# Kernel tuning notes

Measured on AMD Instinct MI355X. Metric: run time of the kernel, lower is better.

Reference implementation:

```python
import jax, jax.numpy as jnp
import numpy as np

B, N, T, H = 64, 15, 256, 128
TEMP = 1.0


def setup_inputs() -> dict:
    key = jax.random.key(0)
    ks = jax.random.split(key, 5)
    node_output = jax.random.normal(ks[0], (B, T, H), jnp.float32)
    neigh_output = jax.random.normal(ks[1], (B, N, T, H), jnp.float32)
    # causal-style mask: True = masked (t' > t); guarantees no fully-masked row
    attn_mask = jnp.broadcast_to(jnp.triu(jnp.ones((T, T), bool), k=1), (B, T, T))
    xav = (2.0 / (H + H)) ** 0.5  # xavier_normal std for square HxH
    Wq = jax.random.normal(ks[2], (H, H), jnp.float32) * xav
    Wk = jax.random.normal(ks[3], (H, H), jnp.float32) * xav
    Wv = jax.random.normal(ks[4], (H, H), jnp.float32) * xav
    z = jnp.zeros((H,), jnp.float32)  # biases init to 0 in init_params
    return dict(node_output=node_output, neigh_output=neigh_output,
                neighbors_number=N, attn_mask=attn_mask,
                Wq=Wq, bq=z, Wk=Wk, bk=z, Wv=Wv, bv=z)


def reference(node_output, neigh_output, neighbors_number, attn_mask,
              Wq, bq, Wk, bk, Wv, bv):
    b, t, h = node_output.shape
    n = neigh_output.shape[1]
    # key/value sequence: self node followed by its n neighbors -> [B, N+1, T, H]
    kv = jnp.concatenate([node_output[:, None], neigh_output], axis=1)
    # Linear (torch convention y = x W^T + b); query repeat collapses to single proj
    q = node_output @ Wq.T + bq                      # [B, T, H]
    k = kv @ Wk.T + bk                               # [B, N+1, T, H]
    v = kv.reshape(b, (n + 1) * t, h) @ Wv.T + bv    # [B, (N+1)*T, H]
    # scores: each query attends separately to every (source, timestep) key
    S = jnp.einsum('bth,bnsh->bnts', q, k)           # [B, N+1, T, T]
    # S_norm computed on the PRE-mask scores (original norms S.data before fill)
    S_norm = jnp.linalg.norm(S.reshape(b, -1), axis=-1)  # [B]
    S = jnp.where(attn_mask[:, None, :, :], -jnp.inf, S)
    S = jnp.transpose(S, (0, 2, 1, 3)) / TEMP        # [B, T, N+1, T]
    # joint softmax over all (N+1)*T keys at once
    A = jax.nn.softmax(S.reshape(b, t, (n + 1) * t), axis=-1)
    out = jnp.einsum('btk,bkh->bth', A, v)           # [B, T, H]
    return out, A.reshape(b, t, n + 1, t), S_norm
```

## Files before the change

### kernel.cpp

```cpp
#include <hip/hip_runtime.h>
#include <math.h>


constexpr int BB   = 64;
constexpr int TT   = 256;
constexpr int HH   = 128;
constexpr int KEYS = 4096;
constexpr int LDK  = 136;
constexpr int LDV  = 72;

typedef __attribute__((ext_vector_type(8)))  __bf16 bf16x8;
typedef __attribute__((ext_vector_type(16))) float  f32x16;
typedef unsigned short ushort_t;

__device__ __forceinline__ float4 ld4(const float* p) {
  return *reinterpret_cast<const float4*>(p);
}
__device__ __forceinline__ ushort_t f2bf(float x) {
  union { __bf16 b; ushort_t u; } c; c.b = (__bf16)x; return c.u;
}
__device__ __forceinline__ float bf2f(ushort_t h) {
  return __uint_as_float(((unsigned)h) << 16);
}
__device__ __forceinline__ void splitf(float x, ushort_t& h, ushort_t& l) {
  h = f2bf(x);
  l = f2bf(x - bf2f(h));
}
__device__ __forceinline__ f32x16 zero16() {
  f32x16 z;
  #pragma unroll
  for (int i = 0; i < 16; ++i) z[i] = 0.f;
  return z;
}
__device__ __forceinline__ f32x16 mfma3(bf16x8 ahi, bf16x8 alo,
                                        bf16x8 bhi, bf16x8 blo, f32x16 c) {
  c = __builtin_amdgcn_mfma_f32_32x32x16_bf16(ahi, bhi, c, 0, 0, 0);
  c = __builtin_amdgcn_mfma_f32_32x32x16_bf16(ahi, blo, c, 0, 0, 0);
  c = __builtin_amdgcn_mfma_f32_32x32x16_bf16(alo, bhi, c, 0, 0, 0);
  return c;
}

__global__ __launch_bounds__(256) void prep_w_kernel(
    const float* __restrict__ Wq, const float* __restrict__ Wk,
    const float* __restrict__ Wv,
    ushort_t* __restrict__ wqh, ushort_t* __restrict__ wql,
    ushort_t* __restrict__ wkh, ushort_t* __restrict__ wkl,
    ushort_t* __restrict__ wvh, ushort_t* __restrict__ wvl)
{
  int i = blockIdx.x * 256 + threadIdx.x;
  if (i >= HH * HH) return;
  ushort_t h, l;
  splitf(Wq[i], h, l); wqh[i] = h; wql[i] = l;
  splitf(Wk[i], h, l); wkh[i] = h; wkl[i] = l;
  splitf(Wv[i], h, l); wvh[i] = h; wvl[i] = l;
}

template<bool DOV>
__global__ __launch_bounds__(256, 2) void proj_kernel(
    const float* __restrict__ node, const float* __restrict__ neigh,
    const ushort_t* __restrict__ W1h, const ushort_t* __restrict__ W1l,
    const float* __restrict__ b1,
    const ushort_t* __restrict__ WVh, const ushort_t* __restrict__ WVl,
    const float* __restrict__ bV,
    ushort_t* __restrict__ yh, ushort_t* __restrict__ yl,
    ushort_t* __restrict__ v_t, int mode)
{
  __shared__ ushort_t xh[128 * LDK];
  __shared__ ushort_t xl[128 * LDK];
  const int tid = threadIdx.x;
  const long r0 = (long)blockIdx.x * 128;

  #pragma unroll
  for (int i = 0; i < 16; ++i) {
    int slot = tid + 256 * i;
    int row = slot >> 5, h0 = (slot & 31) << 2;
    long r = r0 + row;
    const float* src;
    if (mode == 0) {
      src = node + r * HH;
    } else {
      long bb = r >> 12;
      int  n  = (int)((r >> 8) & 15);
      int  t  = (int)(r & 255);
      src = (n == 0) ? (node + (bb * TT + t) * HH)
                     : (neigh + ((bb * 15 + (n - 1)) * (long)TT + t) * HH);
    }
    float4 xv = ld4(src + h0);
    ushort_t h0h, h0l, h1h, h1l, h2h, h2l, h3h, h3l;
    splitf(xv.x, h0h, h0l); splitf(xv.y, h1h, h1l);
    splitf(xv.z, h2h, h2l); splitf(xv.w, h3h, h3l);
    *reinterpret_cast<uint2*>(&xh[row * LDK + h0]) =
        make_uint2((unsigned)h0h | ((unsigned)h1h << 16),
                   (unsigned)h2h | ((unsigned)h3h << 16));
    *reinterpret_cast<uint2*>(&xl[row * LDK + h0]) =
        make_uint2((unsigned)h0l | ((unsigned)h1l << 16),
                   (unsigned)h2l | ((unsigned)h3l << 16));
  }
  __syncthreads();

  const int l = tid & 63, w = tid >> 6, g = l >> 5, lane31 = l & 31;
  const int j = 32 * w + lane31;

  f32x16 accK[4];
  #pragma unroll
  for (int kt = 0; kt < 4; ++kt) accK[kt] = zero16();
  f32x16 accV[4];
  if constexpr (DOV) {
    #pragma unroll
    for (int kt = 0; kt < 4; ++kt) accV[kt] = zero16();
  }

  #pragma unroll
  for (int hs = 0; hs < 8; ++hs) {
    const int ho = 16 * hs + 8 * g;
    bf16x8 wh = *reinterpret_cast<const bf16x8*>(W1h + j * HH + ho);
    bf16x8 wl = *reinterpret_cast<const bf16x8*>(W1l + j * HH + ho);
    bf16x8 xhf[4], xlf[4];
    #pragma unroll
    for (int rt = 0; rt < 4; ++rt) {
      xhf[rt] = *reinterpret_cast<const bf16x8*>(&xh[(32 * rt + lane31) * LDK + ho]);
      xlf[rt] = *reinterpret_cast<const bf16x8*>(&xl[(32 * rt + lane31) * LDK + ho]);
    }
    #pragma unroll
    for (int rt = 0; rt < 4; ++rt)
      accK[rt] = mfma3(xhf[rt], xlf[rt], wh, wl, accK[rt]);
    if constexpr (DOV) {
      bf16x8 vh = *reinterpret_cast<const bf16x8*>(WVh + j * HH + ho);
      bf16x8 vl = *reinterpret_cast<const bf16x8*>(WVl + j * HH + ho);
      #pragma unroll
      for (int rt = 0; rt < 4; ++rt)
        accV[rt] = mfma3(vh, vl, xhf[rt], xlf[rt], accV[rt]);
    }
  }

  const float bK = b1[j];
  #pragma unroll
  for (int kt = 0; kt < 4; ++kt) {
    #pragma unroll
    for (int reg = 0; reg < 16; ++reg) {
      int rm = (reg & 3) + 8 * (reg >> 2) + 4 * g;
      long r = r0 + 32 * kt + rm;
      ushort_t h, lo_;
      splitf(accK[kt][reg] + bK, h, lo_);
      yh[r * HH + j] = h;
      yl[r * HH + j] = lo_;
    }
  }
  if constexpr (DOV) {
    const int bidx = (int)(r0 >> 12);
    const int key0 = (int)(r0 & (KEYS - 1));
    float bvr[16];
    #pragma unroll
    for (int reg = 0; reg < 16; ++reg)
      bvr[reg] = bV[32 * w + (reg & 3) + 8 * (reg >> 2) + 4 * g];
    #pragma unroll
    for (int kt = 0; kt < 4; ++kt) {
      #pragma unroll
      for (int reg = 0; reg < 16; ++reg) {
        int rm = (reg & 3) + 8 * (reg >> 2) + 4 * g;
        int jrow = 32 * w + rm;
        v_t[((long)(bidx * HH + jrow)) * KEYS + key0 + 32 * kt + lane31] =
            f2bf(accV[kt][reg] + bvr[reg]);
      }
    }
  }
}

__global__ __launch_bounds__(128, 2) void passA_kernel(
    const ushort_t* __restrict__ q_hi, const ushort_t* __restrict__ q_lo,
    const ushort_t* __restrict__ k_hi, const ushort_t* __restrict__ k_lo,
    float* __restrict__ m_part, float* __restrict__ l_part,
    float* __restrict__ ssq_part)
{
  __shared__ ushort_t Khi[64 * LDK];
  __shared__ ushort_t Klo[64 * LDK];
  const int tid = threadIdx.x, l = tid & 63, w = tid >> 6;
  const int g = (l >> 5) & 1, lane31 = l & 31;
  const int p = blockIdx.x;
  const int xcd = p & 7, slot = p >> 3;
  const int pair = xcd * 32 + (slot >> 2);
  const int tq = slot & 3;
  const int b = pair >> 2, ks = pair & 3;
  const int t0 = tq * 64;

  bf16x8 qhi[8], qlo[8];
  {
    const long qb = ((long)(b * TT + t0 + 32 * w + lane31)) * HH;
    #pragma unroll
    for (int hs = 0; hs < 8; ++hs) {
      qhi[hs] = *reinterpret_cast<const bf16x8*>(q_hi + qb + 16 * hs + 8 * g);
      qlo[hs] = *reinterpret_cast<const bf16x8*>(q_lo + qb + 16 * hs + 8 * g);
    }
  }

  float mreg[16], lreg[16], ssq = 0.f;
  #pragma unroll
  for (int r = 0; r < 16; ++r) { mreg[r] = -1e30f; lreg[r] = 0.f; }

  for (int kt = 0; kt < 16; ++kt) {
    const int kb = ks * 1024 + kt * 64;
    __syncthreads();
    #pragma unroll
    for (int i = 0; i < 8; ++i) {
      int slot2 = i * 128 + tid;
      int row = slot2 >> 4, c0 = (slot2 & 15) << 3;
      const long gsrc = ((long)(b * KEYS + kb + row)) * HH + c0;
      *reinterpret_cast<uint4*>(&Khi[row * LDK + c0]) =
          *reinterpret_cast<const uint4*>(k_hi + gsrc);
      *reinterpret_cast<uint4*>(&Klo[row * LDK + c0]) =
          *reinterpret_cast<const uint4*>(k_lo + gsrc);
    }
    __syncthreads();

    f32x16 acc0 = zero16(), acc1 = zero16();
    #pragma unroll
    for (int hs = 0; hs < 8; ++hs) {
      const int ho = 16 * hs + 8 * g;
      bf16x8 kh0 = *reinterpret_cast<const bf16x8*>(&Khi[lane31 * LDK + ho]);
      bf16x8 kl0 = *reinterpret_cast<const bf16x8*>(&Klo[lane31 * LDK + ho]);
      bf16x8 kh1 = *reinterpret_cast<const bf16x8*>(&Khi[(32 + lane31) * LDK + ho]);
      bf16x8 kl1 = *reinterpret_cast<const bf16x8*>(&Klo[(32 + lane31) * LDK + ho]);
      acc0 = mfma3(qhi[hs], qlo[hs], kh0, kl0, acc0);
      acc1 = mfma3(qhi[hs], qlo[hs], kh1, kl1, acc1);
    }

    const int st0 = (kb + lane31) & 255;
    const int st1 = (kb + 32 + lane31) & 255;
    #pragma unroll
    for (int reg = 0; reg < 16; ++reg) {
      const int tr = t0 + 32 * w + (reg & 3) + 8 * (reg >> 2) + 4 * g;
      float s0 = acc0[reg], s1 = acc1[reg];
      ssq = fmaf(s0, s0, fmaf(s1, s1, ssq));
      bool msk0 = st0 > tr, msk1 = st1 > tr;
      float v0 = msk0 ? -1e30f : s0;
      float v1 = msk1 ? -1e30f : s1;
      float mn = fmaxf(mreg[reg], fmaxf(v0, v1));
      float sc = __expf(mreg[reg] - mn);
      float p0 = msk0 ? 0.f : __expf(s0 - mn);
      float p1 = msk1 ? 0.f : __expf(s1 - mn);
      lreg[reg] = fmaf(lreg[reg], sc, p0 + p1);
      mreg[reg] = mn;
    }
  }

  #pragma unroll
  for (int reg = 0; reg < 16; ++reg) {
    #pragma unroll
    for (int off = 1; off < 32; off <<= 1) {
      float mo = __shfl_xor(mreg[reg], off);
      float lo = __shfl_xor(lreg[reg], off);
      float mn = fmaxf(mreg[reg], mo);
      lreg[reg] = lreg[reg] * __expf(mreg[reg] - mn) + lo * __expf(mo - mn);
      mreg[reg] = mn;
    }
  }
  if (lane31 == 0) {
    #pragma unroll
    for (int reg = 0; reg < 16; ++reg) {
      const int tr = t0 + 32 * w + (reg & 3) + 8 * (reg >> 2) + 4 * g;
      m_part[ks * (BB * TT) + b * TT + tr] = mreg[reg];
      l_part[ks * (BB * TT) + b * TT + tr] = lreg[reg];
    }
  }
  #pragma unroll
  for (int off = 1; off < 64; off <<= 1) ssq += __shfl_xor(ssq, off);
  __syncthreads();
  float* red = reinterpret_cast<float*>(Khi);
  if (l == 0) red[w] = ssq;
  __syncthreads();
  if (tid == 0) ssq_part[b * 16 + tq * 4 + ks] = red[0] + red[1];
}

__global__ void merge_ml_kernel(const float* __restrict__ m_part,
                                const float* __restrict__ l_part,
                                float* __restrict__ m_ws,
                                float* __restrict__ l_ws)
{
  int idx = blockIdx.x * 256 + threadIdx.x;
  if (idx >= BB * TT) return;
  float m = -1e30f;
  #pragma unroll
  for (int k = 0; k < 4; ++k) m = fmaxf(m, m_part[k * (BB * TT) + idx]);
  float lsum = 0.f;
  #pragma unroll
  for (int k = 0; k < 4; ++k)
    lsum += l_part[k * (BB * TT) + idx] * __expf(m_part[k * (BB * TT) + idx] - m);
  m_ws[idx] = m;
  l_ws[idx] = lsum;
}

__global__ __launch_bounds__(256, 2) void passB_kernel(
    const ushort_t* __restrict__ q_hi, const ushort_t* __restrict__ q_lo,
    const ushort_t* __restrict__ k_hi, const ushort_t* __restrict__ k_lo,
    const ushort_t* __restrict__ v_t,
    const float* __restrict__ m_ws, const float* __restrict__ l_ws,
    float* __restrict__ A_out, float* __restrict__ opart)
{
  __shared__ ushort_t Khi[64 * LDK];
  __shared__ ushort_t Klo[64 * LDK];
  __shared__ ushort_t Vt[128 * LDV];
  __shared__ ushort_t As[64 * LDV];
  const int tid = threadIdx.x, l = tid & 63, w = tid >> 6;
  const int g = (l >> 5) & 1, lane31 = l & 31;
  const int wt = w & 1, wk = w >> 1;
  const int p = blockIdx.x;
  const int xcd = p & 7, slot = p >> 3;
  const int pair = xcd * 16 + (slot >> 2);
  const int tq = slot & 3;
  const int b = pair >> 1, ksb = pair & 1;
  const int t0 = tq * 64;

  bf16x8 qhi[8], qlo[8];
  {
    const long qb = ((long)(b * TT + t0 + 32 * wt + lane31)) * HH;
    #pragma unroll
    for (int hs = 0; hs < 8; ++hs) {
      qhi[hs] = *reinterpret_cast<const bf16x8*>(q_hi + qb + 16 * hs + 8 * g);
      qlo[hs] = *reinterpret_cast<const bf16x8*>(q_lo + qb + 16 * hs + 8 * g);
    }
  }
  float mreg[16], rinv[16];
  #pragma unroll
  for (int reg = 0; reg < 16; ++reg) {
    const int tr = t0 + 32 * wt + (reg & 3) + 8 * (reg >> 2) + 4 * g;
    mreg[reg] = m_ws[b * TT + tr];
    rinv[reg] = 1.0f / l_ws[b * TT + tr];
  }
  f32x16 o0 = zero16(), o1 = zero16();

  for (int kt = 0; kt < 32; ++kt) {
    const int kb = ksb * 2048 + kt * 64;
    __syncthreads();
    #pragma unroll
    for (int i = 0; i < 4; ++i) {
      int slot2 = i * 256 + tid;
      int row = slot2 >> 4, c0 = (slot2 & 15) << 3;
      const long gsrc = ((long)(b * KEYS + kb + row)) * HH + c0;
      *reinterpret_cast<uint4*>(&Khi[row * LDK + c0]) =
          *reinterpret_cast<const uint4*>(k_hi + gsrc);
      *reinterpret_cast<uint4*>(&Klo[row * LDK + c0]) =
          *reinterpret_cast<const uint4*>(k_lo + gsrc);
    }
    #pragma unroll
    for (int i = 0; i < 4; ++i) {
      int slot2 = i * 256 + tid;
      int hh = slot2 >> 3, k0 = (slot2 & 7) << 3;
      *reinterpret_cast<uint4*>(&Vt[hh * LDV + k0]) =
          *reinterpret_cast<const uint4*>(
              v_t + ((long)(b * HH + hh)) * KEYS + kb + k0);
    }
    __syncthreads();

    f32x16 acc = zero16();
    #pragma unroll
    for (int hs = 0; hs < 8; ++hs) {
      const int ho = 16 * hs + 8 * g;
      bf16x8 kh = *reinterpret_cast<const bf16x8*>(
          &Khi[(32 * wk + lane31) * LDK + ho]);
      bf16x8 kl = *reinterpret_cast<const bf16x8*>(
          &Klo[(32 * wk + lane31) * LDK + ho]);
      acc = mfma3(qhi[hs], qlo[hs], kh, kl, acc);
    }

    const int key = kb + 32 * wk + lane31;
    const int st = key & 255;
    #pragma unroll
    for (int reg = 0; reg < 16; ++reg) {
      const int rl = 32 * wt + (reg & 3) + 8 * (reg >> 2) + 4 * g;
      const int tr = t0 + rl;
      float a = (st <= tr) ? __expf(acc[reg] - mreg[reg]) * rinv[reg] : 0.f;
      A_out[((long)(b * TT + tr)) * KEYS + key] = a;
      As[rl * LDV + 32 * wk + lane31] = f2bf(a);
    }
    __syncthreads();

    #pragma unroll
    for (int ksx = 0; ksx < 4; ++ksx) {
      const int ko = 16 * ksx + 8 * g;
      bf16x8 af = *reinterpret_cast<const bf16x8*>(
          &As[(32 * wt + lane31) * LDV + ko]);
      bf16x8 v0 = *reinterpret_cast<const bf16x8*>(
          &Vt[(64 * wk + lane31) * LDV + ko]);
      bf16x8 v1 = *reinterpret_cast<const bf16x8*>(
          &Vt[(64 * wk + 32 + lane31) * LDV + ko]);
      o0 = __builtin_amdgcn_mfma_f32_32x32x16_bf16(af, v0, o0, 0, 0, 0);
      o1 = __builtin_amdgcn_mfma_f32_32x32x16_bf16(af, v1, o1, 0, 0, 0);
    }
  }

  #pragma unroll
  for (int reg = 0; reg < 16; ++reg) {
    const int tr = t0 + 32 * wt + (reg & 3) + 8 * (reg >> 2) + 4 * g;
    long base = (long)ksb * (BB * TT * HH) + ((long)(b * TT + tr)) * HH + 64 * wk;
    opart[base + lane31]      = o0[reg];
    opart[base + 32 + lane31] = o1[reg];
  }
}

__global__ void reduce_out_kernel(const float* __restrict__ opart,
                                  float* __restrict__ out)
{
  int i = blockIdx.x * 256 + threadIdx.x;
  const int n4 = BB * TT * HH / 4;
  if (i >= n4) return;
  const float4* p0 = reinterpret_cast<const float4*>(opart);
  const float4* p1 = reinterpret_cast<const float4*>(opart + BB * TT * HH);
  float4 a = p0[i], c = p1[i];
  a.x += c.x; a.y += c.y; a.z += c.z; a.w += c.w;
  *reinterpret_cast<float4*>(out + 4 * (long)i) = a;
}

__global__ void finalize_kernel(const float* __restrict__ ssq_part,
                                float* __restrict__ S_norm)
{
  int b = threadIdx.x;
  if (b < BB) {
    float s = 0.f;
    #pragma unroll
    for (int i = 0; i < 16; ++i) s += ssq_part[b * 16 + i];
    S_norm[b] = sqrtf(s);
  }
}

extern "C" void kernel_launch(void* const* d_in, const int* in_sizes, int n_in,
                              void* d_out, int out_size, void* d_ws, size_t ws_size,
                              hipStream_t stream)
{
  const float* node  = (const float*)d_in[0];
  const float* neigh = (const float*)d_in[1];
  const float* Wq = (const float*)d_in[4];
  const float* bq = (const float*)d_in[5];
  const float* Wk = (const float*)d_in[6];
  const float* bk = (const float*)d_in[7];
  const float* Wv = (const float*)d_in[8];
  const float* bv = (const float*)d_in[9];

  float* out    = (float*)d_out;
  float* A_out  = out + (long)BB * TT * HH;
  float* S_norm = A_out + (long)BB * TT * KEYS;

  ushort_t* q_hi = (ushort_t*)d_ws;
  ushort_t* q_lo = q_hi + (long)BB * TT * HH;
  ushort_t* k_hi = q_lo + (long)BB * TT * HH;
  ushort_t* k_lo = k_hi + (long)BB * KEYS * HH;
  ushort_t* v_t  = k_lo + (long)BB * KEYS * HH;
  ushort_t* wqh  = v_t + (long)BB * HH * KEYS;
  ushort_t* wql  = wqh + HH * HH;
  ushort_t* wkh  = wql + HH * HH;
  ushort_t* wkl  = wkh + HH * HH;
  ushort_t* wvh  = wkl + HH * HH;
  ushort_t* wvl  = wvh + HH * HH;
  float* m_part = (float*)(wvl + HH * HH);
  float* l_part = m_part + 4 * BB * TT;
  float* ssq_part = l_part + 4 * BB * TT;
  float* opart = ssq_part + 1024;
  float* m_ws  = opart + 2L * BB * TT * HH;
  float* l_ws  = m_ws + BB * TT;

  prep_w_kernel<<<dim3((HH * HH + 255) / 256), dim3(256), 0, stream>>>(
      Wq, Wk, Wv, wqh, wql, wkh, wkl, wvh, wvl);
  proj_kernel<false><<<dim3(BB * TT / 128), dim3(256), 0, stream>>>(
      node, neigh, wqh, wql, bq, wvh, wvl, bv, q_hi, q_lo, v_t, 0);
  proj_kernel<true><<<dim3(BB * KEYS / 128), dim3(256), 0, stream>>>(
      node, neigh, wkh, wkl, bk, wvh, wvl, bv, k_hi, k_lo, v_t, 1);
  passA_kernel<<<dim3(BB * 16), dim3(128), 0, stream>>>(
      q_hi, q_lo, k_hi, k_lo, m_part, l_part, ssq_part);
  merge_ml_kernel<<<dim3((BB * TT + 255) / 256), dim3(256), 0, stream>>>(
      m_part, l_part, m_ws, l_ws);
  passB_kernel<<<dim3(BB * 8), dim3(256), 0, stream>>>(
      q_hi, q_lo, k_hi, k_lo, v_t, m_ws, l_ws, A_out, opart);
  reduce_out_kernel<<<dim3((BB * TT * HH / 4 + 255) / 256), dim3(256), 0, stream>>>(
      opart, out);
  finalize_kernel<<<dim3(1), dim3(64), 0, stream>>>(ssq_part, S_norm);
}
```

Before: 385.0 us.

## Load K fragments directly from global, drop K LDS staging, raise occupancy

Both attention passes now read K hi/lo fragments straight from global memory into MFMA operands instead of staging them in shared memory. This removes the K LDS buffers and a barrier pair per tile. In passB the V tile is prefetched into registers before the QK MFMAs and written to LDS only after the scores are computed. Launch bounds go from 2 to 3 blocks per CU to use the freed LDS. The cost is more scattered global loads per lane and higher register pressure, plus possible redundant K reads across waves.

Result: slower. 600.8 us (+56.1%).

```diff
diff --git a/kernel.cpp b/kernel.cpp
--- a/kernel.cpp
+++ b/kernel.cpp
@@ -166,14 +166,13 @@
   }
 }
 
-__global__ __launch_bounds__(128, 2) void passA_kernel(
+__global__ __launch_bounds__(128, 3) void passA_kernel(
     const ushort_t* __restrict__ q_hi, const ushort_t* __restrict__ q_lo,
     const ushort_t* __restrict__ k_hi, const ushort_t* __restrict__ k_lo,
     float* __restrict__ m_part, float* __restrict__ l_part,
     float* __restrict__ ssq_part)
 {
-  __shared__ ushort_t Khi[64 * LDK];
-  __shared__ ushort_t Klo[64 * LDK];
+  __shared__ float red[2];
   const int tid = threadIdx.x, l = tid & 63, w = tid >> 6;
   const int g = (l >> 5) & 1, lane31 = l & 31;
   const int p = blockIdx.x;
@@ -199,27 +198,17 @@
 
   for (int kt = 0; kt < 16; ++kt) {
     const int kb = ks * 1024 + kt * 64;
-    __syncthreads();
-    #pragma unroll
-    for (int i = 0; i < 8; ++i) {
-      int slot2 = i * 128 + tid;
-      int row = slot2 >> 4, c0 = (slot2 & 15) << 3;
-      const long gsrc = ((long)(b * KEYS + kb + row)) * HH + c0;
-      *reinterpret_cast<uint4*>(&Khi[row * LDK + c0]) =
-          *reinterpret_cast<const uint4*>(k_hi + gsrc);
-      *reinterpret_cast<uint4*>(&Klo[row * LDK + c0]) =
-          *reinterpret_cast<const uint4*>(k_lo + gsrc);
-    }
-    __syncthreads();
+    const long kb0 = ((long)(b * KEYS + kb + lane31)) * HH + 8 * g;
+    const long kb1 = kb0 + 32L * HH;
 
     f32x16 acc0 = zero16(), acc1 = zero16();
     #pragma unroll
     for (int hs = 0; hs < 8; ++hs) {
-      const int ho = 16 * hs + 8 * g;
-      bf16x8 kh0 = *reinterpret_cast<const bf16x8*>(&Khi[lane31 * LDK + ho]);
-      bf16x8 kl0 = *reinterpret_cast<const bf16x8*>(&Klo[lane31 * LDK + ho]);
-      bf16x8 kh1 = *reinterpret_cast<const bf16x8*>(&Khi[(32 + lane31) * LDK + ho]);
-      bf16x8 kl1 = *reinterpret_cast<const bf16x8*>(&Klo[(32 + lane31) * LDK + ho]);
+      const int ho = 16 * hs;
+      bf16x8 kh0 = *reinterpret_cast<const bf16x8*>(k_hi + kb0 + ho);
+      bf16x8 kl0 = *reinterpret_cast<const bf16x8*>(k_lo + kb0 + ho);
+      bf16x8 kh1 = *reinterpret_cast<const bf16x8*>(k_hi + kb1 + ho);
+      bf16x8 kl1 = *reinterpret_cast<const bf16x8*>(k_lo + kb1 + ho);
       acc0 = mfma3(qhi[hs], qlo[hs], kh0, kl0, acc0);
       acc1 = mfma3(qhi[hs], qlo[hs], kh1, kl1, acc1);
     }
@@ -264,8 +253,6 @@
   }
   #pragma unroll
   for (int off = 1; off < 64; off <<= 1) ssq += __shfl_xor(ssq, off);
-  __syncthreads();
-  float* red = reinterpret_cast<float*>(Khi);
   if (l == 0) red[w] = ssq;
   __syncthreads();
   if (tid == 0) ssq_part[b * 16 + tq * 4 + ks] = red[0] + red[1];
@@ -289,15 +276,13 @@
   l_ws[idx] = lsum;
 }
 
-__global__ __launch_bounds__(256, 2) void passB_kernel(
+__global__ __launch_bounds__(256, 3) void passB_kernel(
     const ushort_t* __restrict__ q_hi, const ushort_t* __restrict__ q_lo,
     const ushort_t* __restrict__ k_hi, const ushort_t* __restrict__ k_lo,
     const ushort_t* __restrict__ v_t,
     const float* __restrict__ m_ws, const float* __restrict__ l_ws,
     float* __restrict__ A_out, float* __restrict__ opart)
 {
-  __shared__ ushort_t Khi[64 * LDK];
-  __shared__ ushort_t Klo[64 * LDK];
   __shared__ ushort_t Vt[128 * LDV];
   __shared__ ushort_t As[64 * LDV];
   const int tid = threadIdx.x, l = tid & 63, w = tid >> 6;
@@ -330,47 +315,60 @@
 
   for (int kt = 0; kt < 32; ++kt) {
     const int kb = ksb * 2048 + kt * 64;
-    __syncthreads();
-    #pragma unroll
-    for (int i = 0; i < 4; ++i) {
-      int slot2 = i * 256 + tid;
-      int row = slot2 >> 4, c0 = (slot2 & 15) << 3;
-      const long gsrc = ((long)(b * KEYS + kb + row)) * HH + c0;
-      *reinterpret_cast<uint4*>(&Khi[row * LDK + c0]) =
-          *reinterpret_cast<const uint4*>(k_hi + gsrc);
-      *reinterpret_cast<uint4*>(&Klo[row * LDK + c0]) =
-          *reinterpret_cast<const uint4*>(k_lo + gsrc);
-    }
-    #pragma unroll
-    for (int i = 0; i < 4; ++i) {
-      int slot2 = i * 256 + tid;
-      int hh = slot2 >> 3, k0 = (slot2 & 7) << 3;
-      *reinterpret_cast<uint4*>(&Vt[hh * LDV + k0]) =
-          *reinterpret_cast<const uint4*>(
-              v_t + ((long)(b * HH + hh)) * KEYS + kb + k0);
-    }
-    __syncthreads();
+
+    uint4 rvt0, rvt1, rvt2, rvt3;
+    {
+      int s2 = tid;
+      rvt0 = *reinterpret_cast<const uint4*>(
+          v_t + ((long)(b * HH + (s2 >> 3))) * KEYS + kb + ((s2 & 7) << 3));
+      s2 = 256 + tid;
+      rvt1 = *reinterpret_cast<const uint4*>(
+          v_t + ((long)(b * HH + (s2 >> 3))) * KEYS + kb + ((s2 & 7) << 3));
+      s2 = 512 + tid;
+      rvt2 = *reinterpret_cast<const uint4*>(
+          v_t + ((long)(b * HH + (s2 >> 3))) * KEYS + kb + ((s2 & 7) << 3));
+      s2 = 768 + tid;
+      rvt3 = *reinterpret_cast<const uint4*>(
+          v_t + ((long)(b * HH + (s2 >> 3))) * KEYS + kb + ((s2 & 7) << 3));
+    }
 
     f32x16 acc = zero16();
+    const long kbase = ((long)(b * KEYS + kb + 32 * wk + lane31)) * HH + 8 * g;
     #pragma unroll
     for (int hs = 0; hs < 8; ++hs) {
-      const int ho = 16 * hs + 8 * g;
-      bf16x8 kh = *reinterpret_cast<const bf16x8*>(
-          &Khi[(32 * wk + lane31) * LDK + ho]);
-      bf16x8 kl = *reinterpret_cast<const bf16x8*>(
-          &Klo[(32 * wk + lane31) * LDK + ho]);
+      bf16x8 kh = *reinterpret_cast<const bf16x8*>(k_hi + kbase + 16 * hs);
+      bf16x8 kl = *reinterpret_cast<const bf16x8*>(k_lo + kbase + 16 * hs);
       acc = mfma3(qhi[hs], qlo[hs], kh, kl, acc);
     }
 
     const int key = kb + 32 * wk + lane31;
     const int st = key & 255;
+    float av[16];
     #pragma unroll
     for (int reg = 0; reg < 16; ++reg) {
       const int rl = 32 * wt + (reg & 3) + 8 * (reg >> 2) + 4 * g;
       const int tr = t0 + rl;
       float a = (st <= tr) ? __expf(acc[reg] - mreg[reg]) * rinv[reg] : 0.f;
       A_out[((long)(b * TT + tr)) * KEYS + key] = a;
-      As[rl * LDV + 32 * wk + lane31] = f2bf(a);
+      av[reg] = a;
+    }
+
+    __syncthreads();
+
+    #pragma unroll
+    for (int reg = 0; reg < 16; ++reg) {
+      const int rl = 32 * wt + (reg & 3) + 8 * (reg >> 2) + 4 * g;
+      As[rl * LDV + 32 * wk + lane31] = f2bf(av[reg]);
+    }
+    {
+      int s2 = tid;
+      *reinterpret_cast<uint4*>(&Vt[(s2 >> 3) * LDV + ((s2 & 7) << 3)]) = rvt0;
+      s2 = 256 + tid;
+      *reinterpret_cast<uint4*>(&Vt[(s2 >> 3) * LDV + ((s2 & 7) << 3)]) = rvt1;
+      s2 = 512 + tid;
+      *reinterpret_cast<uint4*>(&Vt[(s2 >> 3) * LDV + ((s2 & 7) << 3)]) = rvt2;
+      s2 = 768 + tid;
+      *reinterpret_cast<uint4*>(&Vt[(s2 >> 3) * LDV + ((s2 & 7) << 3)]) = rvt3;
     }
     __syncthreads();
 
```

## Split passB keys four ways, halve K LDS tile, prefetch via registers

Applied to the files above, without the earlier changes.

The passB attention-output kernel now splits each batch's 4096 keys across four blocks instead of two, doubling the grid to 1024 blocks. The launch bound rises to three blocks per CU. The K tile in shared memory is halved along H and loaded in two phases, with global loads staged through registers so the second half's fetch overlaps the first half's MFMAs. The large A output uses nontemporal stores. The cost is four partial-output buffers, which the reduce kernel must now sum, plus more barriers per tile and higher register pressure.

Result: slower. 443.3 us (+15.2%).

```diff
diff --git a/kernel.cpp b/kernel.cpp
--- a/kernel.cpp
+++ b/kernel.cpp
@@ -7,6 +7,7 @@
 constexpr int HH   = 128;
 constexpr int KEYS = 4096;
 constexpr int LDK  = 136;
+constexpr int LDH  = 72;
 constexpr int LDV  = 72;
 
 typedef __attribute__((ext_vector_type(8)))  __bf16 bf16x8;
@@ -289,15 +290,15 @@
   l_ws[idx] = lsum;
 }
 
-__global__ __launch_bounds__(256, 2) void passB_kernel(
+__global__ __launch_bounds__(256, 3) void passB_kernel(
     const ushort_t* __restrict__ q_hi, const ushort_t* __restrict__ q_lo,
     const ushort_t* __restrict__ k_hi, const ushort_t* __restrict__ k_lo,
     const ushort_t* __restrict__ v_t,
     const float* __restrict__ m_ws, const float* __restrict__ l_ws,
     float* __restrict__ A_out, float* __restrict__ opart)
 {
-  __shared__ ushort_t Khi[64 * LDK];
-  __shared__ ushort_t Klo[64 * LDK];
+  __shared__ ushort_t Khi[64 * LDH];
+  __shared__ ushort_t Klo[64 * LDH];
   __shared__ ushort_t Vt[128 * LDV];
   __shared__ ushort_t As[64 * LDV];
   const int tid = threadIdx.x, l = tid & 63, w = tid >> 6;
@@ -305,9 +306,9 @@
   const int wt = w & 1, wk = w >> 1;
   const int p = blockIdx.x;
   const int xcd = p & 7, slot = p >> 3;
-  const int pair = xcd * 16 + (slot >> 2);
+  const int pair = xcd * 32 + (slot >> 2);
   const int tq = slot & 3;
-  const int b = pair >> 1, ksb = pair & 1;
+  const int b = pair >> 2, ks = pair & 3;
   const int t0 = tq * 64;
 
   bf16x8 qhi[8], qlo[8];
@@ -328,38 +329,61 @@
   }
   f32x16 o0 = zero16(), o1 = zero16();
 
-  for (int kt = 0; kt < 32; ++kt) {
-    const int kb = ksb * 2048 + kt * 64;
-    __syncthreads();
-    #pragma unroll
-    for (int i = 0; i < 4; ++i) {
-      int slot2 = i * 256 + tid;
-      int row = slot2 >> 4, c0 = (slot2 & 15) << 3;
-      const long gsrc = ((long)(b * KEYS + kb + row)) * HH + c0;
-      *reinterpret_cast<uint4*>(&Khi[row * LDK + c0]) =
-          *reinterpret_cast<const uint4*>(k_hi + gsrc);
-      *reinterpret_cast<uint4*>(&Klo[row * LDK + c0]) =
-          *reinterpret_cast<const uint4*>(k_lo + gsrc);
-    }
-    #pragma unroll
-    for (int i = 0; i < 4; ++i) {
-      int slot2 = i * 256 + tid;
-      int hh = slot2 >> 3, k0 = (slot2 & 7) << 3;
-      *reinterpret_cast<uint4*>(&Vt[hh * LDV + k0]) =
-          *reinterpret_cast<const uint4*>(
-              v_t + ((long)(b * HH + hh)) * KEYS + kb + k0);
-    }
-    __syncthreads();
+  const int srow = tid >> 3;
+  const int scol = (tid & 7) << 3;
+
+  for (int kt = 0; kt < 16; ++kt) {
+    const int kb = ks * 1024 + kt * 64;
+    const long kgbase = ((long)(b * KEYS + kb)) * HH;
+    const long vgbase = ((long)b * HH) * KEYS + kb;
+
+    uint4 rkh0 = *reinterpret_cast<const uint4*>(k_hi + kgbase + (long)srow * HH + scol);
+    uint4 rkh1 = *reinterpret_cast<const uint4*>(k_hi + kgbase + (long)(srow + 32) * HH + scol);
+    uint4 rkl0 = *reinterpret_cast<const uint4*>(k_lo + kgbase + (long)srow * HH + scol);
+    uint4 rkl1 = *reinterpret_cast<const uint4*>(k_lo + kgbase + (long)(srow + 32) * HH + scol);
+    uint4 rvt0 = *reinterpret_cast<const uint4*>(v_t + vgbase + (long)srow * KEYS + scol);
+    uint4 rvt1 = *reinterpret_cast<const uint4*>(v_t + vgbase + (long)(srow + 32) * KEYS + scol);
+    uint4 rvt2 = *reinterpret_cast<const uint4*>(v_t + vgbase + (long)(srow + 64) * KEYS + scol);
+    uint4 rvt3 = *reinterpret_cast<const uint4*>(v_t + vgbase + (long)(srow + 96) * KEYS + scol);
+
+    __syncthreads();
+    *reinterpret_cast<uint4*>(&Khi[srow * LDH + scol]) = rkh0;
+    *reinterpret_cast<uint4*>(&Khi[(srow + 32) * LDH + scol]) = rkh1;
+    *reinterpret_cast<uint4*>(&Klo[srow * LDH + scol]) = rkl0;
+    *reinterpret_cast<uint4*>(&Klo[(srow + 32) * LDH + scol]) = rkl1;
+    *reinterpret_cast<uint4*>(&Vt[srow * LDV + scol]) = rvt0;
+    *reinterpret_cast<uint4*>(&Vt[(srow + 32) * LDV + scol]) = rvt1;
+    *reinterpret_cast<uint4*>(&Vt[(srow + 64) * LDV + scol]) = rvt2;
+    *reinterpret_cast<uint4*>(&Vt[(srow + 96) * LDV + scol]) = rvt3;
+    __syncthreads();
+
+    uint4 skh0 = *reinterpret_cast<const uint4*>(k_hi + kgbase + (long)srow * HH + 64 + scol);
+    uint4 skh1 = *reinterpret_cast<const uint4*>(k_hi + kgbase + (long)(srow + 32) * HH + 64 + scol);
+    uint4 skl0 = *reinterpret_cast<const uint4*>(k_lo + kgbase + (long)srow * HH + 64 + scol);
+    uint4 skl1 = *reinterpret_cast<const uint4*>(k_lo + kgbase + (long)(srow + 32) * HH + 64 + scol);
 
     f32x16 acc = zero16();
     #pragma unroll
-    for (int hs = 0; hs < 8; ++hs) {
+    for (int hs = 0; hs < 4; ++hs) {
       const int ho = 16 * hs + 8 * g;
-      bf16x8 kh = *reinterpret_cast<const bf16x8*>(
-          &Khi[(32 * wk + lane31) * LDK + ho]);
-      bf16x8 kl = *reinterpret_cast<const bf16x8*>(
-          &Klo[(32 * wk + lane31) * LDK + ho]);
+      bf16x8 kh = *reinterpret_cast<const bf16x8*>(&Khi[(32 * wk + lane31) * LDH + ho]);
+      bf16x8 kl = *reinterpret_cast<const bf16x8*>(&Klo[(32 * wk + lane31) * LDH + ho]);
       acc = mfma3(qhi[hs], qlo[hs], kh, kl, acc);
+    }
+
+    __syncthreads();
+    *reinterpret_cast<uint4*>(&Khi[srow * LDH + scol]) = skh0;
+    *reinterpret_cast<uint4*>(&Khi[(srow + 32) * LDH + scol]) = skh1;
+    *reinterpret_cast<uint4*>(&Klo[srow * LDH + scol]) = skl0;
+    *reinterpret_cast<uint4*>(&Klo[(srow + 32) * LDH + scol]) = skl1;
+    __syncthreads();
+
+    #pragma unroll
+    for (int hs = 0; hs < 4; ++hs) {
+      const int ho = 16 * hs + 8 * g;
+      bf16x8 kh = *reinterpret_cast<const bf16x8*>(&Khi[(32 * wk + lane31) * LDH + ho]);
+      bf16x8 kl = *reinterpret_cast<const bf16x8*>(&Klo[(32 * wk + lane31) * LDH + ho]);
+      acc = mfma3(qhi[4 + hs], qlo[4 + hs], kh, kl, acc);
     }
 
     const int key = kb + 32 * wk + lane31;
@@ -369,7 +393,7 @@
       const int rl = 32 * wt + (reg & 3) + 8 * (reg >> 2) + 4 * g;
       const int tr = t0 + rl;
       float a = (st <= tr) ? __expf(acc[reg] - mreg[reg]) * rinv[reg] : 0.f;
-      A_out[((long)(b * TT + tr)) * KEYS + key] = a;
+      __builtin_nontemporal_store(a, A_out + ((long)(b * TT + tr)) * KEYS + key);
       As[rl * LDV + 32 * wk + lane31] = f2bf(a);
     }
     __syncthreads();
@@ -391,7 +415,7 @@
   #pragma unroll
   for (int reg = 0; reg < 16; ++reg) {
     const int tr = t0 + 32 * wt + (reg & 3) + 8 * (reg >> 2) + 4 * g;
-    long base = (long)ksb * (BB * TT * HH) + ((long)(b * TT + tr)) * HH + 64 * wk;
+    long base = (long)ks * (BB * TT * HH) + ((long)(b * TT + tr)) * HH + 64 * wk;
     opart[base + lane31]      = o0[reg];
     opart[base + 32 + lane31] = o1[reg];
   }
@@ -403,10 +427,16 @@
   int i = blockIdx.x * 256 + threadIdx.x;
   const int n4 = BB * TT * HH / 4;
   if (i >= n4) return;
+  const long stride = (long)BB * TT * HH;
   const float4* p0 = reinterpret_cast<const float4*>(opart);
-  const float4* p1 = reinterpret_cast<const float4*>(opart + BB * TT * HH);
-  float4 a = p0[i], c = p1[i];
-  a.x += c.x; a.y += c.y; a.z += c.z; a.w += c.w;
+  const float4* p1 = reinterpret_cast<const float4*>(opart + stride);
+  const float4* p2 = reinterpret_cast<const float4*>(opart + 2 * stride);
+  const float4* p3 = reinterpret_cast<const float4*>(opart + 3 * stride);
+  float4 a = p0[i], c = p1[i], d = p2[i], e = p3[i];
+  a.x += c.x + d.x + e.x;
+  a.y += c.y + d.y + e.y;
+  a.z += c.z + d.z + e.z;
+  a.w += c.w + d.w + e.w;
   *reinterpret_cast<float4*>(out + 4 * (long)i) = a;
 }
 
@@ -454,7 +484,7 @@
   float* l_part = m_part + 4 * BB * TT;
   float* ssq_part = l_part + 4 * BB * TT;
   float* opart = ssq_part + 1024;
-  float* m_ws  = opart + 2L * BB * TT * HH;
+  float* m_ws  = opart + 4L * BB * TT * HH;
   float* l_ws  = m_ws + BB * TT;
 
   prep_w_kernel<<<dim3((HH * HH + 255) / 256), dim3(256), 0, stream>>>(
@@ -467,7 +497,7 @@
       q_hi, q_lo, k_hi, k_lo, m_part, l_part, ssq_part);
   merge_ml_kernel<<<dim3((BB * TT + 255) / 256), dim3(256), 0, stream>>>(
       m_part, l_part, m_ws, l_ws);
-  passB_kernel<<<dim3(BB * 8), dim3(256), 0, stream>>>(
+  passB_kernel<<<dim3(BB * 16), dim3(256), 0, stream>>>(
       q_hi, q_lo, k_hi, k_lo, v_t, m_ws, l_ws, A_out, opart);
   reduce_out_kernel<<<dim3((BB * TT * HH / 4 + 255) / 256), dim3(256), 0, stream>>>(
       opart, out);
```
